# Kernel tuning notes

Hardware: AMD Instinct MI355X
Metric: run time of the kernel (lower is better)

The kernel has to match this reference:

```python
import jax, jax.numpy as jnp
import numpy as np

N_NODES = 50000
N_EDGES = 800000
IN_DIM = 128
HID = 128
LATENT = 64
N_LAYERS = 3
N_GRAPHS = 256
BN_EPS = 1e-5


def setup_inputs() -> dict:
    key = jax.random.key(0)
    ks = jax.random.split(key, 12)
    x = jax.random.normal(ks[0], (N_NODES, IN_DIM), dtype=jnp.float32)
    edge_index = jax.random.randint(ks[1], (2, N_EDGES), 0, N_NODES, dtype=jnp.int32)
    batch = jnp.sort(jax.random.randint(ks[2], (N_NODES,), 0, N_GRAPHS, dtype=jnp.int32))
    s = 1.0 / np.sqrt(HID)
    # stacked per-layer SAGEConv params: lin_l (neighbor path, with bias), lin_r (root path)
    Wl = jax.random.uniform(ks[3], (N_LAYERS, HID, HID), jnp.float32, -s, s)
    bl = jax.random.uniform(ks[4], (N_LAYERS, HID), jnp.float32, -s, s)
    Wr = jax.random.uniform(ks[5], (N_LAYERS, HID, HID), jnp.float32, -s, s)
    gamma = jnp.ones((HID,), jnp.float32)
    beta = jnp.zeros((HID,), jnp.float32)
    fcW = jax.random.uniform(ks[6], (HID, LATENT), jnp.float32, -s, s)
    fcb = jax.random.uniform(ks[7], (LATENT,), jnp.float32, -s, s)
    return {"x": x, "edge_index": edge_index, "batch": batch, "Wl": Wl, "bl": bl,
            "Wr": Wr, "gamma": gamma, "beta": beta, "fcW": fcW, "fcb": fcb}


def _sage_conv(x, src, dst, Wl_i, bl_i, Wr_i):
    # mean-aggregate source features into target nodes (PyG SAGEConv, aggr='mean')
    agg = jax.ops.segment_sum(x[src], dst, num_segments=N_NODES)  # [N, D]
    cnt = jax.ops.segment_sum(jnp.ones((src.shape[0],), x.dtype), dst, num_segments=N_NODES)
    mean = agg / jnp.maximum(cnt, 1.0)[:, None]
    return mean @ Wl_i + bl_i + x @ Wr_i


def reference(x, edge_index, batch, Wl, bl, Wr, gamma, beta, fcW, fcb):
    src, dst = edge_index[0], edge_index[1]
    h = x
    for i in range(N_LAYERS):
        h = _sage_conv(h, src, dst, Wl[i], bl[i], Wr[i])
        h = jax.nn.relu(h)  # dropout: identity at inference
    # global_add_pool over graphs
    pooled = jax.ops.segment_sum(h, batch, num_segments=N_GRAPHS)  # [G, HID]
    # BatchNorm1d over the graph dimension (batch statistics)
    mu = pooled.mean(axis=0)
    var = pooled.var(axis=0)
    normed = (pooled - mu) * jax.lax.rsqrt(var + BN_EPS) * gamma + beta
    return normed @ fcW + fcb
```

## Files before the change

### kernel.cpp

```cpp
#include <hip/hip_runtime.h>
#include <cstdint>
#include <cstddef>

constexpr int HID = 128;
constexpr int LATENT = 64;
constexpr int BSHIFT = 7;
constexpr int NBUCK_MAX = 512;
constexpr int EPB = 2048;

typedef __attribute__((ext_vector_type(8))) short short8;
typedef __attribute__((ext_vector_type(4))) float f32x4;

__device__ inline unsigned short f2bf(float f) {
    unsigned u = __float_as_uint(f);
    u += 0x7fff + ((u >> 16) & 1);
    return (unsigned short)(u >> 16);
}
__device__ inline unsigned pack_bf16x2(float lo, float hi) {
    unsigned ulo = __float_as_uint(lo);
    unsigned uhi = __float_as_uint(hi);
    ulo += 0x7fff + ((ulo >> 16) & 1);
    uhi += 0x7fff + ((uhi >> 16) & 1);
    return (ulo >> 16) | (uhi & 0xffff0000u);
}

__global__ __launch_bounds__(256) void bhist_k(const int* __restrict__ dst,
                                               int* __restrict__ bucketTotal, int nE, int nbuck) {
    __shared__ int lh[NBUCK_MAX];
    for (int b = threadIdx.x; b < nbuck; b += 256) lh[b] = 0;
    __syncthreads();
    int base = blockIdx.x * EPB;
    int end = min(base + EPB, nE);
    for (int i = base + threadIdx.x; i < end; i += 256)
        atomicAdd(&lh[dst[i] >> BSHIFT], 1);
    __syncthreads();
    for (int b = threadIdx.x; b < nbuck; b += 256) {
        int c = lh[b];
        if (c) atomicAdd(&bucketTotal[b], c);
    }
}

__global__ __launch_bounds__(512) void bscan_k(const int* __restrict__ bucketTotal,
                                               int* __restrict__ bucketStart,
                                               int* __restrict__ bucketFill,
                                               int* __restrict__ row_ptr,
                                               int nbuck, int nE, int nN) {
    __shared__ int part[512];
    int t = threadIdx.x;
    int v = (t < nbuck) ? bucketTotal[t] : 0;
    part[t] = v;
    __syncthreads();
    for (int d = 1; d < 512; d <<= 1) {
        int u = (t >= d) ? part[t - d] : 0;
        __syncthreads();
        if (t >= d) part[t] += u;
        __syncthreads();
    }
    if (t < nbuck) {
        int excl = part[t] - v;
        bucketStart[t] = excl;
        bucketFill[t]  = excl;
    }
    if (t == 0) { bucketStart[nbuck] = nE; row_ptr[nN] = nE; }
}

__global__ __launch_bounds__(256) void bplace_k(const int* __restrict__ src,
                                                const int* __restrict__ dst,
                                                int* __restrict__ bucketFill,
                                                uint2* __restrict__ staged, int nE, int nbuck) {
    __shared__ int lh[NBUCK_MAX];
    __shared__ int lb[NBUCK_MAX];
    for (int b = threadIdx.x; b < nbuck; b += 256) lh[b] = 0;
    __syncthreads();
    int base = blockIdx.x * EPB;
    int end = min(base + EPB, nE);
    for (int i = base + threadIdx.x; i < end; i += 256)
        atomicAdd(&lh[dst[i] >> BSHIFT], 1);
    __syncthreads();
    for (int b = threadIdx.x; b < nbuck; b += 256) {
        int c = lh[b];
        lb[b] = c ? atomicAdd(&bucketFill[b], c) : 0;
        lh[b] = 0;
    }
    __syncthreads();
    for (int i = base + threadIdx.x; i < end; i += 256) {
        int d = dst[i];
        int b = d >> BSHIFT;
        int loc = atomicAdd(&lh[b], 1);
        staged[lb[b] + loc] = make_uint2((unsigned)src[i], (unsigned)d);
    }
}

__global__ __launch_bounds__(256) void sort_bucket_k(const uint2* __restrict__ staged,
                                                     const int* __restrict__ bucketStart,
                                                     int* __restrict__ row_ptr,
                                                     float* __restrict__ inv,
                                                     int* __restrict__ csr_src, int nN) {
    __shared__ int cnt[128];
    __shared__ int rp[128];
    int g = blockIdx.x;
    int beg = bucketStart[g], end = bucketStart[g + 1];
    if (threadIdx.x < 128) cnt[threadIdx.x] = 0;
    __syncthreads();
    for (int i = beg + threadIdx.x; i < end; i += 256)
        atomicAdd(&cnt[staged[i].y & 127], 1);
    __syncthreads();
    if (threadIdx.x < 128) rp[threadIdx.x] = cnt[threadIdx.x];
    __syncthreads();
    #pragma unroll
    for (int d = 1; d < 128; d <<= 1) {
        int v = 0;
        if (threadIdx.x < 128 && threadIdx.x >= d) v = rp[threadIdx.x - d];
        __syncthreads();
        if (threadIdx.x < 128 && threadIdx.x >= d) rp[threadIdx.x] += v;
        __syncthreads();
    }
    if (threadIdx.x < 128) {
        int c = cnt[threadIdx.x];
        int excl = rp[threadIdx.x] - c;
        int node = (g << BSHIFT) + threadIdx.x;
        if (node < nN) {
            row_ptr[node] = beg + excl;
            inv[node] = 1.0f / fmaxf((float)c, 1.0f);
        }
        cnt[threadIdx.x] = excl;
    }
    __syncthreads();
    for (int i = beg + threadIdx.x; i < end; i += 256) {
        uint2 e = staged[i];
        int pos = atomicAdd(&cnt[e.y & 127], 1);
        csr_src[beg + pos] = (int)e.x;
    }
}

__global__ __launch_bounds__(256) void convfuse_k(const float* __restrict__ x,
                                                  const float* __restrict__ Wl,
                                                  const float* __restrict__ Wr,
                                                  unsigned* __restrict__ hx2,
                                                  unsigned short* __restrict__ WT, int n2x) {
    if (blockIdx.x < 384) {
        int idx = blockIdx.x * 256 + threadIdx.x;
        int l = idx / (128 * 256);
        int rem = idx % (128 * 256);
        int n = rem / 256;
        int k = rem % 256;
        float v = (k < 128) ? Wl[(size_t)l * 128 * 128 + (size_t)k * 128 + n]
                            : Wr[(size_t)l * 128 * 128 + (size_t)(k - 128) * 128 + n];
        WT[idx] = f2bf(v);
    } else {
        int i = (blockIdx.x - 384) * 256 + threadIdx.x;
        if (i < n2x) {
            float2 v = ((const float2*)x)[i];
            hx2[i] = pack_bf16x2(v.x, v.y);
        }
    }
}

__global__ __launch_bounds__(256) void gather_k(const int* __restrict__ row_ptr,
                                                const int* __restrict__ csr_src,
                                                const float* __restrict__ inv,
                                                const uint4* __restrict__ h4,
                                                uint4* __restrict__ mean4, int nN) {
    int w = blockIdx.x * 4 + (threadIdx.x >> 6);
    if (w >= nN) return;
    int lane = threadIdx.x & 63;
    int quarter = lane >> 4;
    int col = lane & 15;
    int beg = row_ptr[w], end = row_ptr[w + 1];
    float accA[8] = {}, accB[8] = {}, accC[8] = {}, accD[8] = {};
    for (int base = beg; base < end; base += 64) {
        int navail = min(64, end - base);
        int idx = (lane < navail) ? csr_src[base + lane] : 0;
        for (int j = 0; j < navail; j += 16) {
            int e0 = j + quarter;
            int e1 = j + 4 + quarter;
            int e2 = j + 8 + quarter;
            int e3 = j + 12 + quarter;
            int s0 = __shfl(idx, min(e0, navail - 1), 64);
            int s1 = __shfl(idx, min(e1, navail - 1), 64);
            int s2 = __shfl(idx, min(e2, navail - 1), 64);
            int s3 = __shfl(idx, min(e3, navail - 1), 64);
            uint4 u0 = h4[(size_t)s0 * 16 + col];
            uint4 u1 = h4[(size_t)s1 * 16 + col];
            uint4 u2 = h4[(size_t)s2 * 16 + col];
            uint4 u3 = h4[(size_t)s3 * 16 + col];
            if (e0 < navail) {
                accA[0] += __uint_as_float(u0.x << 16); accA[1] += __uint_as_float(u0.x & 0xffff0000u);
                accA[2] += __uint_as_float(u0.y << 16); accA[3] += __uint_as_float(u0.y & 0xffff0000u);
                accA[4] += __uint_as_float(u0.z << 16); accA[5] += __uint_as_float(u0.z & 0xffff0000u);
                accA[6] += __uint_as_float(u0.w << 16); accA[7] += __uint_as_float(u0.w & 0xffff0000u);
            }
            if (e1 < navail) {
                accB[0] += __uint_as_float(u1.x << 16); accB[1] += __uint_as_float(u1.x & 0xffff0000u);
                accB[2] += __uint_as_float(u1.y << 16); accB[3] += __uint_as_float(u1.y & 0xffff0000u);
                accB[4] += __uint_as_float(u1.z << 16); accB[5] += __uint_as_float(u1.z & 0xffff0000u);
                accB[6] += __uint_as_float(u1.w << 16); accB[7] += __uint_as_float(u1.w & 0xffff0000u);
            }
            if (e2 < navail) {
                accC[0] += __uint_as_float(u2.x << 16); accC[1] += __uint_as_float(u2.x & 0xffff0000u);
                accC[2] += __uint_as_float(u2.y << 16); accC[3] += __uint_as_float(u2.y & 0xffff0000u);
                accC[4] += __uint_as_float(u2.z << 16); accC[5] += __uint_as_float(u2.z & 0xffff0000u);
                accC[6] += __uint_as_float(u2.w << 16); accC[7] += __uint_as_float(u2.w & 0xffff0000u);
            }
            if (e3 < navail) {
                accD[0] += __uint_as_float(u3.x << 16); accD[1] += __uint_as_float(u3.x & 0xffff0000u);
                accD[2] += __uint_as_float(u3.y << 16); accD[3] += __uint_as_float(u3.y & 0xffff0000u);
                accD[4] += __uint_as_float(u3.z << 16); accD[5] += __uint_as_float(u3.z & 0xffff0000u);
                accD[6] += __uint_as_float(u3.w << 16); accD[7] += __uint_as_float(u3.w & 0xffff0000u);
            }
        }
    }
    #pragma unroll
    for (int k = 0; k < 8; ++k) {
        float v = (accA[k] + accB[k]) + (accC[k] + accD[k]);
        v += __shfl_xor(v, 16, 64);
        v += __shfl_xor(v, 32, 64);
        accA[k] = v;
    }
    if (quarter == 0) {
        float iv = inv[w];
        uint4 o;
        o.x = pack_bf16x2(accA[0] * iv, accA[1] * iv);
        o.y = pack_bf16x2(accA[2] * iv, accA[3] * iv);
        o.z = pack_bf16x2(accA[4] * iv, accA[5] * iv);
        o.w = pack_bf16x2(accA[6] * iv, accA[7] * iv);
        mean4[(size_t)w * 16 + col] = o;
    }
}

__global__ __launch_bounds__(256) void sage_mfma_k(
    const unsigned short* __restrict__ mean,
    const unsigned short* __restrict__ h,
    const unsigned short* __restrict__ WT,
    const float* __restrict__ bl,
    unsigned short* __restrict__ out, int nN)
{
    __shared__ unsigned short sB[128 * 256];

    {
        int row = threadIdx.x >> 1, half = threadIdx.x & 1;
        const short8* src = (const short8*)(WT + row * 256 + half * 128);
        int sw = (row & 7) << 2;
        #pragma unroll
        for (int j = 0; j < 16; ++j) {
            int unit = half * 16 + j;
            int unit2 = unit ^ sw;
            *(short8*)(sB + row * 256 + unit2 * 8) = src[j];
        }
    }
    __syncthreads();

    const int wave = threadIdx.x >> 6;
    const int lane = threadIdx.x & 63;
    const int m = lane & 15;
    const int q = lane >> 4;
    const int row = blockIdx.x * 64 + wave * 16 + m;
    const int rowc = min(row, nN - 1);
    const int swm = (m & 7) << 2;

    f32x4 acc[8] = {};
    #pragma unroll
    for (int ks = 0; ks < 8; ++ks) {
        const unsigned short* Aptr = (ks < 4) ? mean : h;
        short8 a = *(const short8*)(Aptr + (size_t)rowc * HID + (ks & 3) * 32 + q * 8);
        #pragma unroll
        for (int t = 0; t < 8; ++t) {
            int unit2 = (ks * 4 + q) ^ swm;
            short8 b = *(const short8*)(sB + (t * 16 + m) * 256 + unit2 * 8);
            acc[t] = __builtin_amdgcn_mfma_f32_16x16x32_bf16(a, b, acc[t], 0, 0, 0);
        }
    }

    int orow_base = blockIdx.x * 64 + wave * 16 + q * 4;
    #pragma unroll
    for (int t = 0; t < 8; ++t) {
        float bias = bl[t * 16 + m];
        #pragma unroll
        for (int r = 0; r < 4; ++r) {
            int orow = orow_base + r;
            if (orow < nN) {
                float v = fmaxf(acc[t][r] + bias, 0.f);
                out[(size_t)orow * HID + t * 16 + m] = f2bf(v);
            }
        }
    }
}

__global__ __launch_bounds__(256) void pool_seg_k(const unsigned* __restrict__ h2,
                                                  const int* __restrict__ batch,
                                                  float* __restrict__ pooled, int nN) {
    int g = blockIdx.x;
    int lo = 0, hi = nN;
    while (lo < hi) { int mid = (lo + hi) >> 1; if (batch[mid] < g) lo = mid + 1; else hi = mid; }
    int beg = lo;
    hi = nN;
    while (lo < hi) { int mid = (lo + hi) >> 1; if (batch[mid] <= g) lo = mid + 1; else hi = mid; }
    int end = lo;

    int lane = threadIdx.x & 63;
    int sub  = threadIdx.x >> 6;
    float s0 = 0.f, s1 = 0.f;
    for (int i = beg + sub; i < end; i += 4) {
        unsigned u = h2[(size_t)i * 64 + lane];
        s0 += __uint_as_float(u << 16);
        s1 += __uint_as_float(u & 0xffff0000u);
    }
    __shared__ float red[4][HID];
    red[sub][2 * lane]     = s0;
    red[sub][2 * lane + 1] = s1;
    __syncthreads();
    if (sub == 0) {
        float v0 = red[0][2 * lane] + red[1][2 * lane] + red[2][2 * lane] + red[3][2 * lane];
        float v1 = red[0][2 * lane + 1] + red[1][2 * lane + 1] + red[2][2 * lane + 1] + red[3][2 * lane + 1];
        pooled[(size_t)g * HID + 2 * lane]     = v0;
        pooled[(size_t)g * HID + 2 * lane + 1] = v1;
    }
}

__global__ __launch_bounds__(1024) void bn_stats_k(const float* __restrict__ pooled,
                                                   const float* __restrict__ gamma,
                                                   const float* __restrict__ beta,
                                                   float* __restrict__ scale,
                                                   float* __restrict__ shift, int nG) {
    __shared__ float rs[8][HID], rs2[8][HID];
    int j = threadIdx.x & (HID - 1);
    int stripe = threadIdx.x >> 7;
    float s = 0.f, s2 = 0.f;
    for (int g = stripe; g < nG; g += 8) {
        float v = pooled[(size_t)g * HID + j];
        s += v; s2 += v * v;
    }
    rs[stripe][j] = s; rs2[stripe][j] = s2;
    __syncthreads();
    if (threadIdx.x < HID) {
        float S = 0.f, S2 = 0.f;
        #pragma unroll
        for (int k = 0; k < 8; ++k) { S += rs[k][j]; S2 += rs2[k][j]; }
        float invG = 1.0f / (float)nG;
        float mu = S * invG;
        float var = S2 * invG - mu * mu;
        float r = rsqrtf(var + 1e-5f) * gamma[j];
        scale[j] = r;
        shift[j] = beta[j] - mu * r;
    }
}

__global__ __launch_bounds__(LATENT) void fc_k(const float* __restrict__ pooled,
                                               const float* __restrict__ scale,
                                               const float* __restrict__ shift,
                                               const float* __restrict__ fcW,
                                               const float* __restrict__ fcb,
                                               float* __restrict__ out, int nG) {
    int g = blockIdx.x;
    int o = threadIdx.x;
    float acc = fcb[o];
    for (int j = 0; j < HID; ++j) {
        float v = pooled[(size_t)g * HID + j] * scale[j] + shift[j];
        acc += v * fcW[(size_t)j * LATENT + o];
    }
    out[(size_t)g * LATENT + o] = acc;
}

extern "C" void kernel_launch(void* const* d_in, const int* in_sizes, int n_in,
                              void* d_out, int out_size, void* d_ws, size_t ws_size,
                              hipStream_t stream) {
    const float* x     = (const float*)d_in[0];
    const int*   ei    = (const int*)d_in[1];
    const int*   batch = (const int*)d_in[2];
    const float* Wl    = (const float*)d_in[3];
    const float* bl    = (const float*)d_in[4];
    const float* Wr    = (const float*)d_in[5];
    const float* gamma = (const float*)d_in[6];
    const float* beta  = (const float*)d_in[7];
    const float* fcW   = (const float*)d_in[8];
    const float* fcb   = (const float*)d_in[9];
    float* out = (float*)d_out;

    const int nN = in_sizes[0] / HID;
    const int nE = in_sizes[1] / 2;
    const int nG = out_size / LATENT;
    const int* src = ei;
    const int* dst = ei + nE;
    const int nbuck = (nN + 127) >> BSHIFT;

    unsigned short* hx   = (unsigned short*)d_ws;
    unsigned short* B1   = hx + (size_t)nN * HID;
    unsigned short* B2   = B1 + (size_t)nN * HID;
    unsigned short* mean = B2 + (size_t)nN * HID;
    unsigned short* WT   = mean + (size_t)nN * HID;
    float* inv    = (float*)(WT + 3 * 128 * 256);
    float* pooled = inv + nN;
    float* scale  = pooled + (size_t)nG * HID;
    float* shift  = scale + HID;
    int*   row_ptr     = (int*)(shift + HID);
    int*   csr_src     = row_ptr + (nN + 1);
    int*   bucketTotal = csr_src + nE;
    int*   bucketStart = bucketTotal + NBUCK_MAX;
    int*   bucketFill  = bucketStart + NBUCK_MAX + 1;
    uint2* staged      = (uint2*)mean;

    const int ebB = (nE + EPB - 1) / EPB;

    hipMemsetAsync(bucketTotal, 0, (size_t)NBUCK_MAX * sizeof(int), stream);
    bhist_k<<<ebB, 256, 0, stream>>>(dst, bucketTotal, nE, nbuck);
    bscan_k<<<1, 512, 0, stream>>>(bucketTotal, bucketStart, bucketFill, row_ptr, nbuck, nE, nN);
    bplace_k<<<ebB, 256, 0, stream>>>(src, dst, bucketFill, staged, nE, nbuck);
    sort_bucket_k<<<nbuck, 256, 0, stream>>>(staged, bucketStart, row_ptr, inv, csr_src, nN);

    const int n2x = nN * HID / 2;
    convfuse_k<<<384 + (n2x + 255) / 256, 256, 0, stream>>>(x, Wl, Wr, (unsigned*)hx, WT, n2x);

    const int gather_blocks = (nN + 3) / 4;
    const int gemm_blocks = (nN + 63) / 64;

    const unsigned short* hcur = hx;
    unsigned short* outs[3] = {B1, B2, B1};
    for (int l = 0; l < 3; ++l) {
        gather_k<<<gather_blocks, 256, 0, stream>>>(row_ptr, csr_src, inv,
                                                    (const uint4*)hcur, (uint4*)mean, nN);
        sage_mfma_k<<<gemm_blocks, 256, 0, stream>>>(mean, hcur,
                                                     WT + (size_t)l * 128 * 256,
                                                     bl + (size_t)l * HID,
                                                     outs[l], nN);
        hcur = outs[l];
    }

    pool_seg_k<<<nG, 256, 0, stream>>>((const unsigned*)hcur, batch, pooled, nN);
    bn_stats_k<<<1, 1024, 0, stream>>>(pooled, gamma, beta, scale, shift, nG);
    fc_k<<<nG, LATENT, 0, stream>>>(pooled, scale, shift, fcW, fcb, out, nG);
}
```

Before: 337.5 us.

## Fuse CSR histogram with conversion and merge BN stats into FC kernel

```diff
diff --git a/kernel.cpp b/kernel.cpp
--- a/kernel.cpp
+++ b/kernel.cpp
@@ -6,7 +6,7 @@
 constexpr int LATENT = 64;
 constexpr int BSHIFT = 7;
 constexpr int NBUCK_MAX = 512;
-constexpr int EPB = 2048;
+constexpr int EPB = 1024;
 
 typedef __attribute__((ext_vector_type(8))) short short8;
 typedef __attribute__((ext_vector_type(4))) float f32x4;
@@ -24,30 +24,57 @@
     return (ulo >> 16) | (uhi & 0xffff0000u);
 }
 
-__global__ __launch_bounds__(256) void bhist_k(const int* __restrict__ dst,
-                                               int* __restrict__ bucketTotal, int nE, int nbuck) {
-    __shared__ int lh[NBUCK_MAX];
-    for (int b = threadIdx.x; b < nbuck; b += 256) lh[b] = 0;
-    __syncthreads();
-    int base = blockIdx.x * EPB;
-    int end = min(base + EPB, nE);
-    for (int i = base + threadIdx.x; i < end; i += 256)
-        atomicAdd(&lh[dst[i] >> BSHIFT], 1);
-    __syncthreads();
-    for (int b = threadIdx.x; b < nbuck; b += 256) {
-        int c = lh[b];
-        if (c) atomicAdd(&bucketTotal[b], c);
-    }
-}
-
-__global__ __launch_bounds__(512) void bscan_k(const int* __restrict__ bucketTotal,
+__global__ __launch_bounds__(256) void stage1_k(const int* __restrict__ dst,
+                                                const float* __restrict__ x,
+                                                const float* __restrict__ Wl,
+                                                const float* __restrict__ Wr,
+                                                int* __restrict__ partial,
+                                                unsigned* __restrict__ hx2,
+                                                unsigned short* __restrict__ WT,
+                                                int nE, int nbuck, int ebB, int n2x) {
+    if (blockIdx.x < (unsigned)ebB) {
+        __shared__ int lh[NBUCK_MAX];
+        for (int b = threadIdx.x; b < nbuck; b += 256) lh[b] = 0;
+        __syncthreads();
+        int base = blockIdx.x * EPB;
+        int end = min(base + EPB, nE);
+        for (int i = base + threadIdx.x; i < end; i += 256)
+            atomicAdd(&lh[dst[i] >> BSHIFT], 1);
+        __syncthreads();
+        int* row = partial + (size_t)blockIdx.x * NBUCK_MAX;
+        for (int b = threadIdx.x; b < nbuck; b += 256) row[b] = lh[b];
+    } else if (blockIdx.x < (unsigned)(ebB + 384)) {
+        int idx = (blockIdx.x - ebB) * 256 + threadIdx.x;
+        int l = idx / (128 * 256);
+        int rem = idx % (128 * 256);
+        int n = rem / 256;
+        int k = rem % 256;
+        float v = (k < 128) ? Wl[(size_t)l * 128 * 128 + (size_t)k * 128 + n]
+                            : Wr[(size_t)l * 128 * 128 + (size_t)(k - 128) * 128 + n];
+        WT[idx] = f2bf(v);
+    } else {
+        int i = (blockIdx.x - ebB - 384) * 256 + threadIdx.x;
+        if (i < n2x) {
+            float2 v = ((const float2*)x)[i];
+            hx2[i] = pack_bf16x2(v.x, v.y);
+        }
+    }
+}
+
+__global__ __launch_bounds__(512) void bscan_k(int* __restrict__ partial,
                                                int* __restrict__ bucketStart,
-                                               int* __restrict__ bucketFill,
                                                int* __restrict__ row_ptr,
-                                               int nbuck, int nE, int nN) {
+                                               int nbuck, int nE, int nN, int ebB) {
     __shared__ int part[512];
     int t = threadIdx.x;
-    int v = (t < nbuck) ? bucketTotal[t] : 0;
+    int run = 0;
+    for (int k = 0; k < ebB; ++k) {
+        int* p = partial + (size_t)k * NBUCK_MAX + t;
+        int c = *p;
+        *p = run;
+        run += c;
+    }
+    int v = (t < nbuck) ? run : 0;
     part[t] = v;
     __syncthreads();
     for (int d = 1; d < 512; d <<= 1) {
@@ -56,17 +83,14 @@
         if (t >= d) part[t] += u;
         __syncthreads();
     }
-    if (t < nbuck) {
-        int excl = part[t] - v;
-        bucketStart[t] = excl;
-        bucketFill[t]  = excl;
-    }
+    if (t < nbuck) bucketStart[t] = part[t] - v;
     if (t == 0) { bucketStart[nbuck] = nE; row_ptr[nN] = nE; }
 }
 
 __global__ __launch_bounds__(256) void bplace_k(const int* __restrict__ src,
                                                 const int* __restrict__ dst,
-                                                int* __restrict__ bucketFill,
+                                                const int* __restrict__ partial,
+                                                const int* __restrict__ bucketStart,
                                                 uint2* __restrict__ staged, int nE, int nbuck) {
     __shared__ int lh[NBUCK_MAX];
     __shared__ int lb[NBUCK_MAX];
@@ -74,14 +98,9 @@
     __syncthreads();
     int base = blockIdx.x * EPB;
     int end = min(base + EPB, nE);
-    for (int i = base + threadIdx.x; i < end; i += 256)
-        atomicAdd(&lh[dst[i] >> BSHIFT], 1);
-    __syncthreads();
-    for (int b = threadIdx.x; b < nbuck; b += 256) {
-        int c = lh[b];
-        lb[b] = c ? atomicAdd(&bucketFill[b], c) : 0;
-        lh[b] = 0;
-    }
+    const int* myPre = partial + (size_t)blockIdx.x * NBUCK_MAX;
+    for (int b = threadIdx.x; b < nbuck; b += 256)
+        lb[b] = bucketStart[b] + myPre[b];
     __syncthreads();
     for (int i = base + threadIdx.x; i < end; i += 256) {
         int d = dst[i];
@@ -130,29 +149,6 @@
         uint2 e = staged[i];
         int pos = atomicAdd(&cnt[e.y & 127], 1);
         csr_src[beg + pos] = (int)e.x;
-    }
-}
-
-__global__ __launch_bounds__(256) void convfuse_k(const float* __restrict__ x,
-                                                  const float* __restrict__ Wl,
-                                                  const float* __restrict__ Wr,
-                                                  unsigned* __restrict__ hx2,
-                                                  unsigned short* __restrict__ WT, int n2x) {
-    if (blockIdx.x < 384) {
-        int idx = blockIdx.x * 256 + threadIdx.x;
-        int l = idx / (128 * 256);
-        int rem = idx % (128 * 256);
-        int n = rem / 256;
-        int k = rem % 256;
-        float v = (k < 128) ? Wl[(size_t)l * 128 * 128 + (size_t)k * 128 + n]
-                            : Wr[(size_t)l * 128 * 128 + (size_t)(k - 128) * 128 + n];
-        WT[idx] = f2bf(v);
-    } else {
-        int i = (blockIdx.x - 384) * 256 + threadIdx.x;
-        if (i < n2x) {
-            float2 v = ((const float2*)x)[i];
-            hx2[i] = pack_bf16x2(v.x, v.y);
-        }
     }
 }
 
@@ -317,48 +313,35 @@
     }
 }
 
-__global__ __launch_bounds__(1024) void bn_stats_k(const float* __restrict__ pooled,
-                                                   const float* __restrict__ gamma,
-                                                   const float* __restrict__ beta,
-                                                   float* __restrict__ scale,
-                                                   float* __restrict__ shift, int nG) {
-    __shared__ float rs[8][HID], rs2[8][HID];
-    int j = threadIdx.x & (HID - 1);
-    int stripe = threadIdx.x >> 7;
-    float s = 0.f, s2 = 0.f;
-    for (int g = stripe; g < nG; g += 8) {
-        float v = pooled[(size_t)g * HID + j];
-        s += v; s2 += v * v;
-    }
-    rs[stripe][j] = s; rs2[stripe][j] = s2;
-    __syncthreads();
-    if (threadIdx.x < HID) {
-        float S = 0.f, S2 = 0.f;
-        #pragma unroll
-        for (int k = 0; k < 8; ++k) { S += rs[k][j]; S2 += rs2[k][j]; }
-        float invG = 1.0f / (float)nG;
-        float mu = S * invG;
-        float var = S2 * invG - mu * mu;
-        float r = rsqrtf(var + 1e-5f) * gamma[j];
-        scale[j] = r;
-        shift[j] = beta[j] - mu * r;
-    }
-}
-
-__global__ __launch_bounds__(LATENT) void fc_k(const float* __restrict__ pooled,
-                                               const float* __restrict__ scale,
-                                               const float* __restrict__ shift,
+__global__ __launch_bounds__(128) void fc_bn_k(const float* __restrict__ pooled,
+                                               const float* __restrict__ gamma,
+                                               const float* __restrict__ beta,
                                                const float* __restrict__ fcW,
                                                const float* __restrict__ fcb,
                                                float* __restrict__ out, int nG) {
+    __shared__ float scaleS[HID], shiftS[HID];
     int g = blockIdx.x;
-    int o = threadIdx.x;
-    float acc = fcb[o];
-    for (int j = 0; j < HID; ++j) {
-        float v = pooled[(size_t)g * HID + j] * scale[j] + shift[j];
-        acc += v * fcW[(size_t)j * LATENT + o];
-    }
-    out[(size_t)g * LATENT + o] = acc;
+    int j = threadIdx.x;
+    float s = 0.f, s2 = 0.f;
+    for (int gg = 0; gg < nG; ++gg) {
+        float v = pooled[(size_t)gg * HID + j];
+        s += v; s2 += v * v;
+    }
+    float invG = 1.0f / (float)nG;
+    float mu = s * invG;
+    float var = s2 * invG - mu * mu;
+    float r = rsqrtf(var + 1e-5f) * gamma[j];
+    scaleS[j] = r;
+    shiftS[j] = beta[j] - mu * r;
+    __syncthreads();
+    if (j < LATENT) {
+        float acc = fcb[j];
+        for (int k = 0; k < HID; ++k) {
+            float v = pooled[(size_t)g * HID + k] * scaleS[k] + shiftS[k];
+            acc += v * fcW[(size_t)k * LATENT + j];
+        }
+        out[(size_t)g * LATENT + j] = acc;
+    }
 }
 
 extern "C" void kernel_launch(void* const* d_in, const int* in_sizes, int n_in,
@@ -382,6 +365,7 @@
     const int* src = ei;
     const int* dst = ei + nE;
     const int nbuck = (nN + 127) >> BSHIFT;
+    const int ebB = (nE + EPB - 1) / EPB;
 
     unsigned short* hx   = (unsigned short*)d_ws;
     unsigned short* B1   = hx + (size_t)nN * HID;
@@ -390,25 +374,20 @@
     unsigned short* WT   = mean + (size_t)nN * HID;
     float* inv    = (float*)(WT + 3 * 128 * 256);
     float* pooled = inv + nN;
-    float* scale  = pooled + (size_t)nG * HID;
-    float* shift  = scale + HID;
-    int*   row_ptr     = (int*)(shift + HID);
+    int*   row_ptr     = (int*)(pooled + (size_t)nG * HID);
     int*   csr_src     = row_ptr + (nN + 1);
-    int*   bucketTotal = csr_src + nE;
-    int*   bucketStart = bucketTotal + NBUCK_MAX;
-    int*   bucketFill  = bucketStart + NBUCK_MAX + 1;
+    int*   bucketStart = csr_src + nE;
+    int*   partial     = bucketStart + NBUCK_MAX + 1;
     uint2* staged      = (uint2*)mean;
 
-    const int ebB = (nE + EPB - 1) / EPB;
-
-    hipMemsetAsync(bucketTotal, 0, (size_t)NBUCK_MAX * sizeof(int), stream);
-    bhist_k<<<ebB, 256, 0, stream>>>(dst, bucketTotal, nE, nbuck);
-    bscan_k<<<1, 512, 0, stream>>>(bucketTotal, bucketStart, bucketFill, row_ptr, nbuck, nE, nN);
-    bplace_k<<<ebB, 256, 0, stream>>>(src, dst, bucketFill, staged, nE, nbuck);
+    const int n2x = nN * HID / 2;
+    const int convx_blocks = (n2x + 255) / 256;
+
+    stage1_k<<<ebB + 384 + convx_blocks, 256, 0, stream>>>(dst, x, Wl, Wr, partial,
+                                                           (unsigned*)hx, WT, nE, nbuck, ebB, n2x);
+    bscan_k<<<1, 512, 0, stream>>>(partial, bucketStart, row_ptr, nbuck, nE, nN, ebB);
+    bplace_k<<<ebB, 256, 0, stream>>>(src, dst, partial, bucketStart, staged, nE, nbuck);
     sort_bucket_k<<<nbuck, 256, 0, stream>>>(staged, bucketStart, row_ptr, inv, csr_src, nN);
-
-    const int n2x = nN * HID / 2;
-    convfuse_k<<<384 + (n2x + 255) / 256, 256, 0, stream>>>(x, Wl, Wr, (unsigned*)hx, WT, n2x);
 
     const int gather_blocks = (nN + 3) / 4;
     const int gemm_blocks = (nN + 63) / 64;
@@ -426,6 +405,5 @@
     }
 
     pool_seg_k<<<nG, 256, 0, stream>>>((const unsigned*)hcur, batch, pooled, nN);
-    bn_stats_k<<<1, 1024, 0, stream>>>(pooled, gamma, beta, scale, shift, nG);
-    fc_k<<<nG, LATENT, 0, stream>>>(pooled, scale, shift, fcW, fcb, out, nG);
-}
+    fc_bn_k<<<nG, 128, 0, stream>>>(pooled, gamma, beta, fcW, fcb, out, nG);
+}
```

New measurement: 534.5 us. 1.58x slower.
